# Performance work log

Measured on AMD Instinct MI355X. Metric: run time of the kernel, lower is better.

The kernel has to match this reference:

```python
import jax, jax.numpy as jnp
import numpy as np


def setup_inputs() -> dict:
    key = jax.random.key(0)
    ks = jax.random.split(key, 9)
    B, Q, K, F, C = 16, 2048, 2048, 128, 2
    q = jax.random.normal(ks[0], (B, Q, F), dtype=jnp.float32)
    k = jax.random.normal(ks[1], (B, K, F), dtype=jnp.float32)
    v = jax.random.normal(ks[2], (B, K, F), dtype=jnp.float32)
    coords_q = jax.random.uniform(ks[3], (B, Q, C), dtype=jnp.float32)
    coords_k = jax.random.uniform(ks[4], (B, K, C), dtype=jnp.float32)
    attn_mask = jax.random.randint(ks[5], (B, Q, K), 0, 2).astype(jnp.bool_)
    alibi_mask = jax.random.randint(ks[6], (B, Q, K), 0, 2).astype(jnp.bool_)
    bias_scale = jax.random.uniform(ks[7], (1,), dtype=jnp.float32)  # nn.Parameter(torch.rand(1))
    running_mean = jnp.ones((1,), dtype=jnp.float32)  # RunningMeanScaler buffer (eval mode)
    return {"q": q, "k": k, "v": v, "coords_q": coords_q, "coords_k": coords_k,
            "attn_mask": attn_mask, "alibi_mask": alibi_mask,
            "bias_scale": bias_scale, "running_mean": running_mean}


def reference(q, k, v, coords_q, coords_k, attn_mask, alibi_mask, bias_scale, running_mean):
    # [b,q,k] attention logits
    scale = jnp.asarray(k.shape[-1], q.dtype) ** -0.5
    weight_logits = jnp.einsum('bqf,bkf->bqk', q, k) * scale
    # pairwise coordinate distances [b,q,k]
    diff = coords_q[:, :, None, :] - coords_k[:, None, :, :]
    distances = jnp.sqrt(jnp.sum(diff * diff, axis=-1))
    scaled_distances = (distances / running_mean) * bias_scale  # broadcast scalars
    masked_distances = jnp.where(alibi_mask, jnp.zeros((), distances.dtype), scaled_distances)
    weights = jax.nn.softmax(weight_logits, axis=-1)
    masked = jnp.where(attn_mask, jnp.zeros((), weights.dtype), weights - masked_distances)
    attention = jnp.einsum('bqk,bkf->bqf', masked, v)
    return attention
```

## Files before the change

kernel.cpp:

```cpp
#include <hip/hip_runtime.h>
#include <stdint.h>

#define B_  16
#define QL  2048
#define KL  2048
#define FD  128
#define BQ  64
#define BK  32
#define NSTEP (KL/BK)

#define KSTR  136
#define VTOFF 4352
#define VTSTR 36
#define BUFS  8960
#define PSTR  40
#define MSTR  36
#define WS_HALF (B_*KL*FD)

typedef __attribute__((ext_vector_type(8))) short bf16x8;
typedef __attribute__((ext_vector_type(4))) float f32x4;
typedef __attribute__((ext_vector_type(4))) int   i32x4;

__device__ __forceinline__ unsigned short f2b(float f) {
  union { float f; unsigned u; } x; x.f = f;
  return (unsigned short)((x.u + 0x8000u) >> 16);
}

__global__ __launch_bounds__(256) void conv_k(const float* __restrict__ kp,
                                              unsigned short* __restrict__ kb) {
  int idx = (blockIdx.x * 256 + threadIdx.x) * 4;
  float4 u = *(const float4*)(kp + idx);
  ushort4 s4; s4.x = f2b(u.x); s4.y = f2b(u.y); s4.z = f2b(u.z); s4.w = f2b(u.w);
  *(ushort4*)(kb + idx) = s4;
}

__global__ __launch_bounds__(256) void conv_vt(const float* __restrict__ vp,
                                               unsigned short* __restrict__ vt) {
  __shared__ float tl[32 * 132];
  const int t = threadIdx.x, b = blockIdx.x >> 6, kt = blockIdx.x & 63;
  const int r = t >> 3, f0 = (t & 7) * 16;
  const float* src = vp + ((long long)(b * KL + kt * 32 + r)) * FD + f0;
  #pragma unroll
  for (int i = 0; i < 4; ++i)
    *(float4*)&tl[r * 132 + f0 + 4 * i] = *(const float4*)(src + 4 * i);
  __syncthreads();
  const int f = t >> 1, half = t & 1;
  bf16x8 o0, o1;
  #pragma unroll
  for (int j = 0; j < 8; ++j)  o0[j] = (short)f2b(tl[(half * 16 + j) * 132 + f]);
  #pragma unroll
  for (int j = 0; j < 8; ++j)  o1[j] = (short)f2b(tl[(half * 16 + 8 + j) * 132 + f]);
  unsigned short* dst = vt + ((long long)((b * 64 + kt) * FD + f)) * 32 + half * 16;
  *(bf16x8*)dst = o0;
  *(bf16x8*)(dst + 8) = o1;
}

__global__ __launch_bounds__(256, 2) void alibi_attn(
    const unsigned short* __restrict__ kbp,
    const unsigned short* __restrict__ vtp,
    const float* __restrict__ qp,
    const float* __restrict__ cqp,
    const float* __restrict__ ckp,
    const int* __restrict__ amp,
    const int* __restrict__ almp,
    const float* __restrict__ bsp,
    const float* __restrict__ rmp,
    float* __restrict__ outp)
{
  __shared__ unsigned short kv[2 * BUFS];
  __shared__ unsigned short plds[4][2][16 * PSTR];
  __shared__ unsigned char  mlds[2][64 * MSTR];

  const int t    = threadIdx.x;
  const int w    = t >> 6;
  const int lane = t & 63;
  const int l15  = lane & 15;
  const int q4   = lane >> 4;

  const int bid  = blockIdx.x;
  const int xcd  = bid & 7, slot = bid >> 3;
  const int b    = (xcd << 1) | (slot >> 5);
  const int qbase = (slot & 31) * BQ;

  const float bscale = bsp[0] / rmp[0];
  const float sl2 = 0.08838834764831845f * 1.44269504089f;

  const int kr_st = t >> 3, kc_st = (t & 7) * 16;
  const int vf_st = t >> 1, vh_st = (t & 1) * 16;
  const int mrow = t >> 2, mcol = (t & 3) * 8;
  const long long mgbase = ((long long)(b * QL + qbase + mrow)) * KL + mcol;
  const int mlo = mrow * MSTR + mcol;

  {
    const float* qg = qp + ((long long)(b * QL + qbase)) * FD;
    #pragma unroll
    for (int i = 0; i < 8; ++i) {
      int idx = t + 256 * i;
      float4 u = ((const float4*)qg)[idx];
      int row = idx >> 5, col = (idx & 31) * 4;
      ushort4 s4; s4.x = f2b(u.x); s4.y = f2b(u.y); s4.z = f2b(u.z); s4.w = f2b(u.w);
      *(ushort4*)&kv[row * KSTR + col] = s4;
    }
  }
  __syncthreads();
  bf16x8 qfrag[4];
  {
    const int m = w * 16 + l15;
    #pragma unroll
    for (int fs = 0; fs < 4; ++fs)
      qfrag[fs] = *(const bf16x8*)&kv[m * KSTR + fs * 32 + q4 * 8];
  }
  float cqx[4], cqy[4];
  #pragma unroll
  for (int r = 0; r < 4; ++r) {
    const int qg_ = qbase + w * 16 + q4 * 4 + r;
    float2 c2 = *(const float2*)(cqp + ((long long)(b * QL + qg_)) * 2);
    cqx[r] = c2.x; cqy[r] = c2.y;
  }
  __syncthreads();

  const unsigned short* kgb = kbp + (long long)b * KL * FD;
  const unsigned short* vgb = vtp + (long long)b * KL * FD;

  float ckx_b[2][2], cky_b[2][2];

  {
    i32x4 a0 = __builtin_nontemporal_load((const i32x4*)(amp + mgbase));
    i32x4 a1 = __builtin_nontemporal_load((const i32x4*)(amp + mgbase + 4));
    i32x4 g0 = __builtin_nontemporal_load((const i32x4*)(almp + mgbase));
    i32x4 g1 = __builtin_nontemporal_load((const i32x4*)(almp + mgbase + 4));
    bf16x8 k0l = *(const bf16x8*)(kgb + kr_st * FD + kc_st);
    bf16x8 k1l = *(const bf16x8*)(kgb + kr_st * FD + kc_st + 8);
    bf16x8 v0l = *(const bf16x8*)(vgb + t * 16);
    bf16x8 v1l = *(const bf16x8*)(vgb + t * 16 + 8);
    #pragma unroll
    for (int s = 0; s < 2; ++s) {
      float2 c2 = *(const float2*)(ckp + ((long long)(b * KL + s * 16 + l15)) * 2);
      ckx_b[0][s] = c2.x; cky_b[0][s] = c2.y;
    }
    unsigned ua = (unsigned)(a0[0] | (a0[1] << 8) | (a0[2] << 16) | (a0[3] << 24));
    unsigned ul = (unsigned)(g0[0] | (g0[1] << 8) | (g0[2] << 16) | (g0[3] << 24));
    *(unsigned*)&mlds[0][mlo] = ua | (ul << 1);
    ua = (unsigned)(a1[0] | (a1[1] << 8) | (a1[2] << 16) | (a1[3] << 24));
    ul = (unsigned)(g1[0] | (g1[1] << 8) | (g1[2] << 16) | (g1[3] << 24));
    *(unsigned*)&mlds[0][mlo + 4] = ua | (ul << 1);
    *(bf16x8*)&kv[kr_st * KSTR + kc_st]     = k0l;
    *(bf16x8*)&kv[kr_st * KSTR + kc_st + 8] = k1l;
    *(bf16x8*)&kv[VTOFF + vf_st * VTSTR + vh_st]     = v0l;
    *(bf16x8*)&kv[VTOFF + vf_st * VTSTR + vh_st + 8] = v1l;
  }
  __syncthreads();

  f32x4 O1[8], O2[8];
  #pragma unroll
  for (int n = 0; n < 8; ++n) {
    O1[n] = (f32x4){0.f, 0.f, 0.f, 0.f};
    O2[n] = (f32x4){0.f, 0.f, 0.f, 0.f};
  }
  float lsum[4] = {0.f, 0.f, 0.f, 0.f};

  #pragma unroll 2
  for (int kt = 0; kt < NSTEP; ++kt) {
    const int cur = kt & 1, nxt = cur ^ 1;
    const unsigned short* kb = kv + cur * BUFS;
    unsigned short*       nb = kv + nxt * BUFS;
    const int ktp = (kt + 1 < NSTEP) ? (kt + 1) : kt;
    const int k0p = ktp * BK;

    i32x4 a0 = __builtin_nontemporal_load((const i32x4*)(amp + mgbase + k0p));
    i32x4 a1 = __builtin_nontemporal_load((const i32x4*)(amp + mgbase + k0p + 4));
    i32x4 g0 = __builtin_nontemporal_load((const i32x4*)(almp + mgbase + k0p));
    i32x4 g1 = __builtin_nontemporal_load((const i32x4*)(almp + mgbase + k0p + 4));
    bf16x8 k0l = *(const bf16x8*)(kgb + (k0p + kr_st) * FD + kc_st);
    bf16x8 k1l = *(const bf16x8*)(kgb + (k0p + kr_st) * FD + kc_st + 8);
    bf16x8 v0l = *(const bf16x8*)(vgb + ktp * (32 * FD) + t * 16);
    bf16x8 v1l = *(const bf16x8*)(vgb + ktp * (32 * FD) + t * 16 + 8);
    #pragma unroll
    for (int s = 0; s < 2; ++s) {
      float2 c2 = *(const float2*)(ckp + ((long long)(b * KL + k0p + s * 16 + l15)) * 2);
      ckx_b[nxt][s] = c2.x; cky_b[nxt][s] = c2.y;
    }

    f32x4 S0 = (f32x4){0.f, 0.f, 0.f, 0.f};
    f32x4 S1 = (f32x4){0.f, 0.f, 0.f, 0.f};
    #pragma unroll
    for (int fs = 0; fs < 4; ++fs) {
      bf16x8 kb0 = *(const bf16x8*)&kb[(l15)      * KSTR + fs * 32 + q4 * 8];
      bf16x8 kb1 = *(const bf16x8*)&kb[(16 + l15) * KSTR + fs * 32 + q4 * 8];
      S0 = __builtin_amdgcn_mfma_f32_16x16x32_bf16(qfrag[fs], kb0, S0, 0, 0, 0);
      S1 = __builtin_amdgcn_mfma_f32_16x16x32_bf16(qfrag[fs], kb1, S1, 0, 0, 0);
    }

    #pragma unroll
    for (int s = 0; s < 2; ++s) {
      const f32x4 Sv = s ? S1 : S0;
      #pragma unroll
      for (int r = 0; r < 4; ++r) {
        unsigned char m = mlds[cur][(w * 16 + q4 * 4 + r) * MSTR + s * 16 + l15];
        float e = __builtin_amdgcn_exp2f(Sv[r] * sl2);
        lsum[r] += e;
        float dx = cqx[r] - ckx_b[cur][s], dy = cqy[r] - cky_b[cur][s];
        float d  = sqrtf(fmaf(dx, dx, dy * dy)) * bscale;
        float wv = (m & 1) ? 0.f : e;
        float tv = m ? 0.f : d;
        const int mm = q4 * 4 + r, c = s * 16 + l15;
        plds[w][0][mm * PSTR + c] = f2b(wv);
        plds[w][1][mm * PSTR + c] = f2b(tv);
      }
    }

    bf16x8 aw = *(const bf16x8*)&plds[w][0][l15 * PSTR + q4 * 8];
    bf16x8 at = *(const bf16x8*)&plds[w][1][l15 * PSTR + q4 * 8];
    #pragma unroll
    for (int n = 0; n < 8; ++n) {
      bf16x8 vb = *(const bf16x8*)&kb[VTOFF + (n * 16 + l15) * VTSTR + q4 * 8];
      O1[n] = __builtin_amdgcn_mfma_f32_16x16x32_bf16(aw, vb, O1[n], 0, 0, 0);
      O2[n] = __builtin_amdgcn_mfma_f32_16x16x32_bf16(at, vb, O2[n], 0, 0, 0);
    }

    unsigned ua = (unsigned)(a0[0] | (a0[1] << 8) | (a0[2] << 16) | (a0[3] << 24));
    unsigned ul = (unsigned)(g0[0] | (g0[1] << 8) | (g0[2] << 16) | (g0[3] << 24));
    *(unsigned*)&mlds[nxt][mlo] = ua | (ul << 1);
    ua = (unsigned)(a1[0] | (a1[1] << 8) | (a1[2] << 16) | (a1[3] << 24));
    ul = (unsigned)(g1[0] | (g1[1] << 8) | (g1[2] << 16) | (g1[3] << 24));
    *(unsigned*)&mlds[nxt][mlo + 4] = ua | (ul << 1);
    *(bf16x8*)&nb[kr_st * KSTR + kc_st]     = k0l;
    *(bf16x8*)&nb[kr_st * KSTR + kc_st + 8] = k1l;
    *(bf16x8*)&nb[VTOFF + vf_st * VTSTR + vh_st]     = v0l;
    *(bf16x8*)&nb[VTOFF + vf_st * VTSTR + vh_st + 8] = v1l;
    __syncthreads();
  }

  #pragma unroll
  for (int off = 1; off < 16; off <<= 1) {
    #pragma unroll
    for (int r = 0; r < 4; ++r) lsum[r] += __shfl_xor(lsum[r], off, 64);
  }
  float linv[4];
  #pragma unroll
  for (int r = 0; r < 4; ++r) linv[r] = 1.0f / lsum[r];

  #pragma unroll
  for (int n = 0; n < 8; ++n) {
    #pragma unroll
    for (int r = 0; r < 4; ++r) {
      const int qg_ = qbase + w * 16 + q4 * 4 + r;
      const int f   = n * 16 + l15;
      float val = O1[n][r] * linv[r] - O2[n][r];
      __builtin_nontemporal_store(val, outp + ((long long)(b * QL + qg_)) * FD + f);
    }
  }
}

extern "C" void kernel_launch(void* const* d_in, const int* in_sizes, int n_in,
                              void* d_out, int out_size, void* d_ws, size_t ws_size,
                              hipStream_t stream) {
  const float* q   = (const float*)d_in[0];
  const float* k   = (const float*)d_in[1];
  const float* v   = (const float*)d_in[2];
  const float* cq  = (const float*)d_in[3];
  const float* ck  = (const float*)d_in[4];
  const int*   am  = (const int*)d_in[5];
  const int*   alm = (const int*)d_in[6];
  const float* bs  = (const float*)d_in[7];
  const float* rm  = (const float*)d_in[8];
  float*       out = (float*)d_out;

  unsigned short* kb = (unsigned short*)d_ws;
  unsigned short* vt = kb + WS_HALF;

  hipLaunchKernelGGL(conv_k,  dim3(WS_HALF / 1024), dim3(256), 0, stream, k, kb);
  hipLaunchKernelGGL(conv_vt, dim3(B_ * 64),        dim3(256), 0, stream, v, vt);

  dim3 grid(B_ * (QL / BQ));
  dim3 block(256);
  hipLaunchKernelGGL(alibi_attn, grid, block, 0, stream,
                     kb, vt, q, cq, ck, am, alm, bs, rm, out);
}
```

Measured before the change: 665.3 us.

## Drop LDS staging for K/V/masks; read MFMA operands directly from global

Removes the double-buffered shared-memory staging of K, V^T and the packed masks, along with the per-step __syncthreads. Each wave now loads its MFMA operands for K and V^T straight from global (L2) memory, reads Q fragments directly from global, and prefetches the mask values into registers one step ahead. The aim is to cut LDS traffic and block-wide barriers. In exchange, the four waves of a block each re-read the same K/V tile, raising global/L2 traffic. The mask loads also become scalar per-element reads, which are less coalesced and use more registers.

```diff
diff --git a/kernel.cpp b/kernel.cpp
--- a/kernel.cpp
+++ b/kernel.cpp
@@ -8,18 +8,11 @@
 #define BQ  64
 #define BK  32
 #define NSTEP (KL/BK)
-
-#define KSTR  136
-#define VTOFF 4352
-#define VTSTR 36
-#define BUFS  8960
 #define PSTR  40
-#define MSTR  36
 #define WS_HALF (B_*KL*FD)
 
 typedef __attribute__((ext_vector_type(8))) short bf16x8;
 typedef __attribute__((ext_vector_type(4))) float f32x4;
-typedef __attribute__((ext_vector_type(4))) int   i32x4;
 
 __device__ __forceinline__ unsigned short f2b(float f) {
   union { float f; unsigned u; } x; x.f = f;
@@ -67,9 +60,7 @@
     const float* __restrict__ rmp,
     float* __restrict__ outp)
 {
-  __shared__ unsigned short kv[2 * BUFS];
   __shared__ unsigned short plds[4][2][16 * PSTR];
-  __shared__ unsigned char  mlds[2][64 * MSTR];
 
   const int t    = threadIdx.x;
   const int w    = t >> 6;
@@ -85,71 +76,45 @@
   const float bscale = bsp[0] / rmp[0];
   const float sl2 = 0.08838834764831845f * 1.44269504089f;
 
-  const int kr_st = t >> 3, kc_st = (t & 7) * 16;
-  const int vf_st = t >> 1, vh_st = (t & 1) * 16;
-  const int mrow = t >> 2, mcol = (t & 3) * 8;
-  const long long mgbase = ((long long)(b * QL + qbase + mrow)) * KL + mcol;
-  const int mlo = mrow * MSTR + mcol;
-
-  {
-    const float* qg = qp + ((long long)(b * QL + qbase)) * FD;
-    #pragma unroll
-    for (int i = 0; i < 8; ++i) {
-      int idx = t + 256 * i;
-      float4 u = ((const float4*)qg)[idx];
-      int row = idx >> 5, col = (idx & 31) * 4;
-      ushort4 s4; s4.x = f2b(u.x); s4.y = f2b(u.y); s4.z = f2b(u.z); s4.w = f2b(u.w);
-      *(ushort4*)&kv[row * KSTR + col] = s4;
-    }
-  }
-  __syncthreads();
   bf16x8 qfrag[4];
   {
-    const int m = w * 16 + l15;
-    #pragma unroll
-    for (int fs = 0; fs < 4; ++fs)
-      qfrag[fs] = *(const bf16x8*)&kv[m * KSTR + fs * 32 + q4 * 8];
+    const float* qrow = qp + ((long long)(b * QL + qbase + w * 16 + l15)) * FD;
+    #pragma unroll
+    for (int fs = 0; fs < 4; ++fs) {
+      float4 u0 = *(const float4*)(qrow + fs * 32 + q4 * 8);
+      float4 u1 = *(const float4*)(qrow + fs * 32 + q4 * 8 + 4);
+      qfrag[fs][0] = (short)f2b(u0.x); qfrag[fs][1] = (short)f2b(u0.y);
+      qfrag[fs][2] = (short)f2b(u0.z); qfrag[fs][3] = (short)f2b(u0.w);
+      qfrag[fs][4] = (short)f2b(u1.x); qfrag[fs][5] = (short)f2b(u1.y);
+      qfrag[fs][6] = (short)f2b(u1.z); qfrag[fs][7] = (short)f2b(u1.w);
+    }
   }
   float cqx[4], cqy[4];
+  long long mrow_base[4];
   #pragma unroll
   for (int r = 0; r < 4; ++r) {
     const int qg_ = qbase + w * 16 + q4 * 4 + r;
     float2 c2 = *(const float2*)(cqp + ((long long)(b * QL + qg_)) * 2);
     cqx[r] = c2.x; cqy[r] = c2.y;
-  }
-  __syncthreads();
+    mrow_base[r] = ((long long)(b * QL + qg_)) * KL;
+  }
 
   const unsigned short* kgb = kbp + (long long)b * KL * FD;
   const unsigned short* vgb = vtp + (long long)b * KL * FD;
 
-  float ckx_b[2][2], cky_b[2][2];
-
-  {
-    i32x4 a0 = __builtin_nontemporal_load((const i32x4*)(amp + mgbase));
-    i32x4 a1 = __builtin_nontemporal_load((const i32x4*)(amp + mgbase + 4));
-    i32x4 g0 = __builtin_nontemporal_load((const i32x4*)(almp + mgbase));
-    i32x4 g1 = __builtin_nontemporal_load((const i32x4*)(almp + mgbase + 4));
-    bf16x8 k0l = *(const bf16x8*)(kgb + kr_st * FD + kc_st);
-    bf16x8 k1l = *(const bf16x8*)(kgb + kr_st * FD + kc_st + 8);
-    bf16x8 v0l = *(const bf16x8*)(vgb + t * 16);
-    bf16x8 v1l = *(const bf16x8*)(vgb + t * 16 + 8);
-    #pragma unroll
-    for (int s = 0; s < 2; ++s) {
-      float2 c2 = *(const float2*)(ckp + ((long long)(b * KL + s * 16 + l15)) * 2);
-      ckx_b[0][s] = c2.x; cky_b[0][s] = c2.y;
-    }
-    unsigned ua = (unsigned)(a0[0] | (a0[1] << 8) | (a0[2] << 16) | (a0[3] << 24));
-    unsigned ul = (unsigned)(g0[0] | (g0[1] << 8) | (g0[2] << 16) | (g0[3] << 24));
-    *(unsigned*)&mlds[0][mlo] = ua | (ul << 1);
-    ua = (unsigned)(a1[0] | (a1[1] << 8) | (a1[2] << 16) | (a1[3] << 24));
-    ul = (unsigned)(g1[0] | (g1[1] << 8) | (g1[2] << 16) | (g1[3] << 24));
-    *(unsigned*)&mlds[0][mlo + 4] = ua | (ul << 1);
-    *(bf16x8*)&kv[kr_st * KSTR + kc_st]     = k0l;
-    *(bf16x8*)&kv[kr_st * KSTR + kc_st + 8] = k1l;
-    *(bf16x8*)&kv[VTOFF + vf_st * VTSTR + vh_st]     = v0l;
-    *(bf16x8*)&kv[VTOFF + vf_st * VTSTR + vh_st + 8] = v1l;
-  }
-  __syncthreads();
+  int   amv[2][8], alv[2][8];
+  float ckxv[2][2], ckyv[2][2];
+  #pragma unroll
+  for (int s = 0; s < 2; ++s) {
+    const int kg = s * 16 + l15;
+    #pragma unroll
+    for (int r = 0; r < 4; ++r) {
+      amv[0][s * 4 + r] = __builtin_nontemporal_load(amp + mrow_base[r] + kg);
+      alv[0][s * 4 + r] = __builtin_nontemporal_load(almp + mrow_base[r] + kg);
+    }
+    float2 c2 = *(const float2*)(ckp + ((long long)(b * KL + kg)) * 2);
+    ckxv[0][s] = c2.x; ckyv[0][s] = c2.y;
+  }
 
   f32x4 O1[8], O2[8];
   #pragma unroll
@@ -162,31 +127,29 @@
   #pragma unroll 2
   for (int kt = 0; kt < NSTEP; ++kt) {
     const int cur = kt & 1, nxt = cur ^ 1;
-    const unsigned short* kb = kv + cur * BUFS;
-    unsigned short*       nb = kv + nxt * BUFS;
+    const int k0  = kt * BK;
     const int ktp = (kt + 1 < NSTEP) ? (kt + 1) : kt;
     const int k0p = ktp * BK;
 
-    i32x4 a0 = __builtin_nontemporal_load((const i32x4*)(amp + mgbase + k0p));
-    i32x4 a1 = __builtin_nontemporal_load((const i32x4*)(amp + mgbase + k0p + 4));
-    i32x4 g0 = __builtin_nontemporal_load((const i32x4*)(almp + mgbase + k0p));
-    i32x4 g1 = __builtin_nontemporal_load((const i32x4*)(almp + mgbase + k0p + 4));
-    bf16x8 k0l = *(const bf16x8*)(kgb + (k0p + kr_st) * FD + kc_st);
-    bf16x8 k1l = *(const bf16x8*)(kgb + (k0p + kr_st) * FD + kc_st + 8);
-    bf16x8 v0l = *(const bf16x8*)(vgb + ktp * (32 * FD) + t * 16);
-    bf16x8 v1l = *(const bf16x8*)(vgb + ktp * (32 * FD) + t * 16 + 8);
     #pragma unroll
     for (int s = 0; s < 2; ++s) {
-      float2 c2 = *(const float2*)(ckp + ((long long)(b * KL + k0p + s * 16 + l15)) * 2);
-      ckx_b[nxt][s] = c2.x; cky_b[nxt][s] = c2.y;
-    }
-
+      const int kg = k0p + s * 16 + l15;
+      #pragma unroll
+      for (int r = 0; r < 4; ++r) {
+        amv[nxt][s * 4 + r] = __builtin_nontemporal_load(amp + mrow_base[r] + kg);
+        alv[nxt][s * 4 + r] = __builtin_nontemporal_load(almp + mrow_base[r] + kg);
+      }
+      float2 c2 = *(const float2*)(ckp + ((long long)(b * KL + kg)) * 2);
+      ckxv[nxt][s] = c2.x; ckyv[nxt][s] = c2.y;
+    }
+
+    const unsigned short* kt_ptr = kgb + (long long)k0 * FD;
     f32x4 S0 = (f32x4){0.f, 0.f, 0.f, 0.f};
     f32x4 S1 = (f32x4){0.f, 0.f, 0.f, 0.f};
     #pragma unroll
     for (int fs = 0; fs < 4; ++fs) {
-      bf16x8 kb0 = *(const bf16x8*)&kb[(l15)      * KSTR + fs * 32 + q4 * 8];
-      bf16x8 kb1 = *(const bf16x8*)&kb[(16 + l15) * KSTR + fs * 32 + q4 * 8];
+      bf16x8 kb0 = *(const bf16x8*)(kt_ptr + (l15)      * FD + fs * 32 + q4 * 8);
+      bf16x8 kb1 = *(const bf16x8*)(kt_ptr + (16 + l15) * FD + fs * 32 + q4 * 8);
       S0 = __builtin_amdgcn_mfma_f32_16x16x32_bf16(qfrag[fs], kb0, S0, 0, 0, 0);
       S1 = __builtin_amdgcn_mfma_f32_16x16x32_bf16(qfrag[fs], kb1, S1, 0, 0, 0);
     }
@@ -196,13 +159,13 @@
       const f32x4 Sv = s ? S1 : S0;
       #pragma unroll
       for (int r = 0; r < 4; ++r) {
-        unsigned char m = mlds[cur][(w * 16 + q4 * 4 + r) * MSTR + s * 16 + l15];
+        int am = amv[cur][s * 4 + r], al = alv[cur][s * 4 + r];
         float e = __builtin_amdgcn_exp2f(Sv[r] * sl2);
         lsum[r] += e;
-        float dx = cqx[r] - ckx_b[cur][s], dy = cqy[r] - cky_b[cur][s];
+        float dx = cqx[r] - ckxv[cur][s], dy = cqy[r] - ckyv[cur][s];
         float d  = sqrtf(fmaf(dx, dx, dy * dy)) * bscale;
-        float wv = (m & 1) ? 0.f : e;
-        float tv = m ? 0.f : d;
+        float wv = am ? 0.f : e;
+        float tv = (am | al) ? 0.f : d;
         const int mm = q4 * 4 + r, c = s * 16 + l15;
         plds[w][0][mm * PSTR + c] = f2b(wv);
         plds[w][1][mm * PSTR + c] = f2b(tv);
@@ -211,24 +174,13 @@
 
     bf16x8 aw = *(const bf16x8*)&plds[w][0][l15 * PSTR + q4 * 8];
     bf16x8 at = *(const bf16x8*)&plds[w][1][l15 * PSTR + q4 * 8];
+    const unsigned short* vt_ptr = vgb + (long long)kt * (BK * FD);
     #pragma unroll
     for (int n = 0; n < 8; ++n) {
-      bf16x8 vb = *(const bf16x8*)&kb[VTOFF + (n * 16 + l15) * VTSTR + q4 * 8];
+      bf16x8 vb = *(const bf16x8*)(vt_ptr + (n * 16 + l15) * 32 + q4 * 8);
       O1[n] = __builtin_amdgcn_mfma_f32_16x16x32_bf16(aw, vb, O1[n], 0, 0, 0);
       O2[n] = __builtin_amdgcn_mfma_f32_16x16x32_bf16(at, vb, O2[n], 0, 0, 0);
     }
-
-    unsigned ua = (unsigned)(a0[0] | (a0[1] << 8) | (a0[2] << 16) | (a0[3] << 24));
-    unsigned ul = (unsigned)(g0[0] | (g0[1] << 8) | (g0[2] << 16) | (g0[3] << 24));
-    *(unsigned*)&mlds[nxt][mlo] = ua | (ul << 1);
-    ua = (unsigned)(a1[0] | (a1[1] << 8) | (a1[2] << 16) | (a1[3] << 24));
-    ul = (unsigned)(g1[0] | (g1[1] << 8) | (g1[2] << 16) | (g1[3] << 24));
-    *(unsigned*)&mlds[nxt][mlo + 4] = ua | (ul << 1);
-    *(bf16x8*)&nb[kr_st * KSTR + kc_st]     = k0l;
-    *(bf16x8*)&nb[kr_st * KSTR + kc_st + 8] = k1l;
-    *(bf16x8*)&nb[VTOFF + vf_st * VTSTR + vh_st]     = v0l;
-    *(bf16x8*)&nb[VTOFF + vf_st * VTSTR + vh_st + 8] = v1l;
-    __syncthreads();
   }
 
   #pragma unroll
```

Result: slower. 800.4 us (+20.3%).
